# Performance work log

Measured on AMD Instinct MI355X. Metric: run time of the kernel, lower is better.

The kernel has to match this reference:

```python
import jax, jax.numpy as jnp
import numpy as np

B, OBS, H, A, E = 131072, 194, 64, 5, 3  # batch, obs dim, hidden, max_action_dim, n event types


def setup_inputs() -> dict:
    key = jax.random.key(0)
    ks = jax.random.split(key, 16)
    s = lambda k, shape, std=0.1: (jax.random.normal(k, shape, dtype=jnp.float32) * std)
    return {
        "x": jax.random.normal(ks[0], (B, OBS), dtype=jnp.float32),
        "action": jax.random.randint(ks[1], (B,), 0, A),
        "W1": s(ks[2], (OBS, H)), "b1": jnp.zeros((H,), jnp.float32),
        "W2": s(ks[3], (H, H)),   "b2": jnp.zeros((H,), jnp.float32),
        "Wh": s(ks[4], (E, H, A), 0.01), "bh": jnp.zeros((E, A), jnp.float32),
        "Wc1": s(ks[5], (OBS, H)), "bc1": jnp.zeros((H,), jnp.float32),
        "Wc2": s(ks[6], (H, H)),   "bc2": jnp.zeros((H,), jnp.float32),
        "Wc3": s(ks[7], (H, 1)),   "bc3": jnp.zeros((1,), jnp.float32),
    }


def reference(x, action, W1, b1, W2, b2, Wh, bh, Wc1, bc1, Wc2, bc2, Wc3, bc3):
    # shared trunk
    feat = jnp.tanh(jnp.tanh(x @ W1 + b1) @ W2 + b2)          # [B, H]
    # route each sample to one of E heads via argmax of first 3 obs dims
    ev = jnp.argmax(x[:, :E], axis=1)                          # [B] int
    all_logits = jnp.einsum('bh,eha->bea', feat, Wh) + bh      # [B, E, A]
    logits = jnp.take_along_axis(
        all_logits, jnp.broadcast_to(ev[:, None, None], (x.shape[0], 1, A)), axis=1
    )[:, 0]                                                    # [B, A]
    logp_all = jax.nn.log_softmax(logits, axis=-1)             # [B, A]
    logp = jnp.take_along_axis(logp_all, action[:, None], axis=1)[:, 0]  # [B]
    entropy = -jnp.sum(jnp.exp(logp_all) * logp_all, axis=-1)  # [B]
    # critic
    value = jnp.tanh(jnp.tanh(x @ Wc1 + bc1) @ Wc2 + bc2) @ Wc3 + bc3    # [B, 1]
    return action, logp, entropy, value
```

## Files before the change

### kernel.cpp

```cpp
#include <hip/hip_runtime.h>
#include <hip/hip_bf16.h>

constexpr int Bt    = 131072;
constexpr int OBS   = 194;

constexpr int W1B_S  = 0;
constexpr int WC1B_S = 14336;
constexpr int W2B_S  = 28672;
constexpr int WC2B_S = 36864;
constexpr int WHB_S  = 45056;
constexpr size_t EVG_B = 98304;
constexpr size_t HG_S  = 131072;

typedef short bf8   __attribute__((ext_vector_type(8)));
typedef float f32x4 __attribute__((ext_vector_type(4)));
typedef unsigned int u32;

__device__ __forceinline__ short f2bs(float f) {
    union { __hip_bfloat16 h; short s; } u;
    u.h = __float2bfloat16(f);
    return u.s;
}
__device__ __forceinline__ float bs2f(short s) {
    union { short s; __hip_bfloat16 h; } u;
    u.s = s;
    return __bfloat162float(u.h);
}
__device__ __forceinline__ u32 pk2(float a, float b) {
    union { __hip_bfloat162 h; u32 u; } r;
    r.h = __float22bfloat162_rn(float2{a, b});
    return r.u;
}
__device__ __forceinline__ float fast_tanh(float v) {
    v = fminf(fmaxf(v, -15.f), 15.f);
    float e = __expf(2.f * v);
    return (e - 1.f) * __builtin_amdgcn_rcpf(e + 1.f);
}
__device__ __forceinline__ void dma16(const void* g, void* s) {
    __builtin_amdgcn_global_load_lds(
        (const __attribute__((address_space(1))) u32*)g,
        (__attribute__((address_space(3))) u32*)s, 16, 0, 0);
}

__global__ void __launch_bounds__(256) prep(
    const float* __restrict__ W1, const float* __restrict__ b1,
    const float* __restrict__ W2, const float* __restrict__ Wh,
    const float* __restrict__ Wc1, const float* __restrict__ bc1,
    const float* __restrict__ Wc2, const float* __restrict__ Wc3,
    short* __restrict__ ws)
{
    const int gid = blockIdx.x * 256 + threadIdx.x;
    const int gsz = gridDim.x * 256;

    for (int i = gid; i < 14336; i += gsz) {
        int j = i & 7, l = (i >> 3) & 63, nt = (i >> 9) & 3, kb = i >> 11;
        int k = kb * 32 + ((l >> 4) << 3) + j;
        int n = nt * 16 + (l & 15);
        short v1 = 0, v2 = 0;
        if (k < OBS) {
            v1 = f2bs(W1[k * 64 + n]);
            v2 = f2bs(Wc1[k * 64 + n]);
        } else if (k == OBS) {
            v1 = f2bs(b1[n]);
            v2 = f2bs(bc1[n]);
        }
        ws[W1B_S + i]  = v1;
        ws[WC1B_S + i] = v2;
    }
    for (int i = gid; i < 8192; i += gsz) {
        int j = i & 7, l = (i >> 3) & 63, nt = (i >> 9) & 3, kb = i >> 11;
        int s = kb * 32 + ((l >> 4) << 3) + j;
        int kp = (s & 3) * 16 + (s >> 2);
        int n = nt * 16 + (l & 15);
        ws[W2B_S + i]  = f2bs(W2[kp * 64 + n]);
        ws[WC2B_S + i] = f2bs(Wc2[kp * 64 + n]);
    }
    for (int i = gid; i < 1024; i += gsz) {
        int j = i & 7, l = (i >> 3) & 63, kb = i >> 9;
        int s = kb * 32 + ((l >> 4) << 3) + j;
        int kp = (s & 3) * 16 + (s >> 2);
        int cc = l & 15;
        float v;
        if (cc == 15) v = Wc3[kp];
        else { int e = cc / 5, a = cc - 5 * e; v = Wh[(e * 64 + kp) * 5 + a]; }
        ws[WHB_S + i] = f2bs(v);
    }
}

constexpr int P1_XS0 = 57344;
constexpr int P1_XSS = 12544;
constexpr int P1_LDS = P1_XS0 + 8 * P1_XSS;

__global__ void __launch_bounds__(512, 2) trunk1(
    const float* __restrict__ x, const short* __restrict__ ws,
    short* __restrict__ hG, unsigned char* __restrict__ evG)
{
    __shared__ __align__(16) char smem[P1_LDS];
    const int t = threadIdx.x;
    const int l = t & 63, q = (t >> 4) & 3, c = t & 15;
    const int wu = __builtin_amdgcn_readfirstlane(t >> 6);

    #pragma unroll
    for (int i = 0; i < 7; ++i) {
        int ch = wu * 7 + i;
        dma16((const char*)ws + ch * 1024 + l * 16, smem + ch * 1024);
    }

    char* xs = smem + P1_XS0 + wu * P1_XSS;
    const int t0 = blockIdx.x * 32 + wu * 4;

    auto stage = [&](int tt) {
        const char* src = (const char*)x + (size_t)tt * 12416;
        #pragma unroll
        for (int ch = 0; ch < 12; ++ch)
            dma16(src + ch * 1024 + l * 16, xs + ch * 1024);
        dma16(src + 11392 + l * 16, xs + 11392);
    };
    stage(t0);

    __syncthreads();

    const bf8* fW1L  = reinterpret_cast<const bf8*>(smem);
    const bf8* fWc1L = reinterpret_cast<const bf8*>(smem + 28672);

    #pragma unroll 1
    for (int i = 0; i < 4; ++i) {
        const int tt = t0 + i;

        if (i) {
            asm volatile("s_waitcnt vmcnt(0)" ::: "memory");
            __builtin_amdgcn_sched_barrier(0);
        }

        union AF { u32 u[4]; bf8 v; } af[7];
        #pragma unroll
        for (int kb = 0; kb < 6; ++kb) {
            #pragma unroll
            for (int j = 0; j < 4; ++j) {
                float2 v = *reinterpret_cast<const float2*>(xs + c * 776 + kb * 128 + q * 32 + j * 8);
                af[kb].u[j] = pk2(v.x, v.y);
            }
        }
        af[6].u[0] = 0; af[6].u[1] = 0; af[6].u[2] = 0; af[6].u[3] = 0;
        if (q == 0) {
            float2 v = *reinterpret_cast<const float2*>(xs + c * 776 + 768);
            af[6].u[0] = pk2(v.x, v.y);
            af[6].u[1] = pk2(1.0f, 0.0f);
        }
        if (l < 16) {
            float2 v01 = *reinterpret_cast<const float2*>(xs + l * 776);
            float  v2  = *reinterpret_cast<const float*>(xs + l * 776 + 8);
            int ev = 0; float b = v01.x;
            if (v01.y > b) { b = v01.y; ev = 1; }
            if (v2 > b) ev = 2;
            evG[tt * 16 + l] = (unsigned char)ev;
        }

        __builtin_amdgcn_sched_barrier(0);
        if (i < 3) stage(tt + 1);
        __builtin_amdgcn_sched_barrier(0);

        f32x4 aa[4], ac[4];
        #pragma unroll
        for (int nt = 0; nt < 4; ++nt) {
            aa[nt] = f32x4{0.f, 0.f, 0.f, 0.f};
            ac[nt] = f32x4{0.f, 0.f, 0.f, 0.f};
        }
        #pragma unroll
        for (int kb = 0; kb < 7; ++kb) {
            bf8 a = af[kb].v;
            #pragma unroll
            for (int nt = 0; nt < 4; ++nt) {
                aa[nt] = __builtin_amdgcn_mfma_f32_16x16x32_bf16(a, fW1L [(kb * 4 + nt) * 64 + l], aa[nt], 0, 0, 0);
                ac[nt] = __builtin_amdgcn_mfma_f32_16x16x32_bf16(a, fWc1L[(kb * 4 + nt) * 64 + l], ac[nt], 0, 0, 0);
            }
        }
        short* hGt = hG + (size_t)tt * 2048;
        #pragma unroll
        for (int r = 0; r < 4; ++r) {
            uint2 pa, pc;
            pa.x = pk2(fast_tanh(aa[0][r]), fast_tanh(aa[1][r]));
            pa.y = pk2(fast_tanh(aa[2][r]), fast_tanh(aa[3][r]));
            pc.x = pk2(fast_tanh(ac[0][r]), fast_tanh(ac[1][r]));
            pc.y = pk2(fast_tanh(ac[2][r]), fast_tanh(ac[3][r]));
            *reinterpret_cast<uint2*>(hGt + (q * 4 + r) * 64 + 4 * c)        = pa;
            *reinterpret_cast<uint2*>(hGt + 1024 + (q * 4 + r) * 64 + 4 * c) = pc;
        }
    }
}

constexpr int F2_W   = 34816;
constexpr int F2_PW  = 5248;
constexpr int F2_LDS = F2_W + 8 * F2_PW;

__global__ void __launch_bounds__(512, 4) head2(
    const int* __restrict__ act_in,
    const float* __restrict__ b2, const float* __restrict__ bc2,
    const float* __restrict__ bh, const float* __restrict__ bc3,
    const short* __restrict__ ws,
    const short* __restrict__ hG, const unsigned char* __restrict__ evG,
    float* __restrict__ out)
{
    __shared__ __align__(16) char smem[F2_LDS];
    const int t = threadIdx.x;
    const int l = t & 63, q = (t >> 4) & 3, c = t & 15;
    const int wu = __builtin_amdgcn_readfirstlane(t >> 6);

    #pragma unroll
    for (int i = 0; i < 5; ++i) {
        int ch = wu + i * 8;
        if (ch < 34)
            dma16((const char*)ws + 57344 + ch * 1024 + l * 16, smem + ch * 1024);
    }

    float b2v[4], bc2v[4];
    #pragma unroll
    for (int nt = 0; nt < 4; ++nt) {
        b2v[nt]  = b2[nt * 16 + c];
        bc2v[nt] = bc2[nt * 16 + c];
    }
    float bhv = (c < 15) ? bh[c] : bc3[0];

    __syncthreads();

    const bf8* fW2L  = reinterpret_cast<const bf8*>(smem);
    const bf8* fWc2L = reinterpret_cast<const bf8*>(smem + 16384);
    const bf8* fWhL  = reinterpret_cast<const bf8*>(smem + 32768);
    short* ha = reinterpret_cast<short*>(smem + F2_W + wu * F2_PW);
    short* hc = ha + 1152;
    short* lw = reinterpret_cast<short*>(smem + F2_W + wu * F2_PW + 4608);
    float* vb = reinterpret_cast<float*>(smem + F2_W + wu * F2_PW + 5184);

    #pragma unroll 1
    for (int i = 0; i < 2; ++i) {
        const int tt = blockIdx.x * 16 + wu * 2 + i;
        const int gm = tt * 16 + c;
        int act = 0, evc = 0;
        if (l < 16) { act = act_in[gm]; evc = evG[gm]; }

        const short* hGt = hG + (size_t)tt * 2048;
        uint2 va[4], vc2[4];
        #pragma unroll
        for (int r = 0; r < 4; ++r) {
            va[r]  = *reinterpret_cast<const uint2*>(hGt + (q * 4 + r) * 64 + 4 * c);
            vc2[r] = *reinterpret_cast<const uint2*>(hGt + 1024 + (q * 4 + r) * 64 + 4 * c);
        }
        #pragma unroll
        for (int r = 0; r < 4; ++r) {
            *reinterpret_cast<uint2*>(&ha[(q * 4 + r) * 72 + 4 * c]) = va[r];
            *reinterpret_cast<uint2*>(&hc[(q * 4 + r) * 72 + 4 * c]) = vc2[r];
        }
        bf8 xa[2], xc[2];
        #pragma unroll
        for (int kb = 0; kb < 2; ++kb) {
            xa[kb] = *reinterpret_cast<const bf8*>(&ha[c * 72 + kb * 32 + q * 8]);
            xc[kb] = *reinterpret_cast<const bf8*>(&hc[c * 72 + kb * 32 + q * 8]);
        }

        f32x4 aa[4], ac[4];
        #pragma unroll
        for (int nt = 0; nt < 4; ++nt) {
            aa[nt] = f32x4{b2v[nt], b2v[nt], b2v[nt], b2v[nt]};
            ac[nt] = f32x4{bc2v[nt], bc2v[nt], bc2v[nt], bc2v[nt]};
        }
        #pragma unroll
        for (int kb = 0; kb < 2; ++kb) {
            #pragma unroll
            for (int nt = 0; nt < 4; ++nt) {
                aa[nt] = __builtin_amdgcn_mfma_f32_16x16x32_bf16(xa[kb], fW2L [(kb * 4 + nt) * 64 + l], aa[nt], 0, 0, 0);
                ac[nt] = __builtin_amdgcn_mfma_f32_16x16x32_bf16(xc[kb], fWc2L[(kb * 4 + nt) * 64 + l], ac[nt], 0, 0, 0);
            }
        }
        #pragma unroll
        for (int r = 0; r < 4; ++r) {
            uint2 pa, pc;
            pa.x = pk2(fast_tanh(aa[0][r]), fast_tanh(aa[1][r]));
            pa.y = pk2(fast_tanh(aa[2][r]), fast_tanh(aa[3][r]));
            pc.x = pk2(fast_tanh(ac[0][r]), fast_tanh(ac[1][r]));
            pc.y = pk2(fast_tanh(ac[2][r]), fast_tanh(ac[3][r]));
            *reinterpret_cast<uint2*>(&ha[(q * 4 + r) * 72 + 4 * c]) = pa;
            *reinterpret_cast<uint2*>(&hc[(q * 4 + r) * 72 + 4 * c]) = pc;
        }

        {
            f32x4 lg = f32x4{bhv, bhv, bhv, bhv};
            f32x4 vv = f32x4{bhv, bhv, bhv, bhv};
            #pragma unroll
            for (int kb = 0; kb < 2; ++kb) {
                bf8 bw = fWhL[kb * 64 + l];
                bf8 fa = *reinterpret_cast<const bf8*>(&ha[c * 72 + kb * 32 + q * 8]);
                bf8 fc = *reinterpret_cast<const bf8*>(&hc[c * 72 + kb * 32 + q * 8]);
                lg = __builtin_amdgcn_mfma_f32_16x16x32_bf16(fa, bw, lg, 0, 0, 0);
                vv = __builtin_amdgcn_mfma_f32_16x16x32_bf16(fc, bw, vv, 0, 0, 0);
            }
            #pragma unroll
            for (int r = 0; r < 4; ++r)
                lw[(q * 4 + r) * 18 + c] = f2bs(lg[r]);
            if (c == 15) {
                #pragma unroll
                for (int r = 0; r < 4; ++r)
                    vb[q * 4 + r] = vv[r];
            }
        }

        if (l < 16) {
            float lg[5];
            #pragma unroll
            for (int a = 0; a < 5; ++a)
                lg[a] = bs2f(lw[c * 18 + evc * 5 + a]);
            float mx = lg[0];
            #pragma unroll
            for (int a = 1; a < 5; ++a) mx = fmaxf(mx, lg[a]);
            float se = 0.f;
            #pragma unroll
            for (int a = 0; a < 5; ++a) se += __expf(lg[a] - mx);
            float lse = __logf(se) + mx;
            float lsel = lg[0];
            #pragma unroll
            for (int a = 1; a < 5; ++a) lsel = (act == a) ? lg[a] : lsel;
            float ent = 0.f;
            #pragma unroll
            for (int a = 0; a < 5; ++a) { float lp = lg[a] - lse; ent -= __expf(lp) * lp; }

            out[gm]          = (float)act;
            out[Bt + gm]     = lsel - lse;
            out[2 * Bt + gm] = ent;
            out[3 * Bt + gm] = vb[c];
        }
    }
}

extern "C" void kernel_launch(void* const* d_in, const int* in_sizes, int n_in,
                              void* d_out, int out_size, void* d_ws, size_t ws_size,
                              hipStream_t stream) {
    const float* x   = (const float*)d_in[0];
    const int*   act = (const int*)  d_in[1];
    const float* W1  = (const float*)d_in[2];
    const float* b1  = (const float*)d_in[3];
    const float* W2  = (const float*)d_in[4];
    const float* b2  = (const float*)d_in[5];
    const float* Wh  = (const float*)d_in[6];
    const float* bh  = (const float*)d_in[7];
    const float* Wc1 = (const float*)d_in[8];
    const float* bc1 = (const float*)d_in[9];
    const float* Wc2 = (const float*)d_in[10];
    const float* bc2 = (const float*)d_in[11];
    const float* Wc3 = (const float*)d_in[12];
    const float* bc3 = (const float*)d_in[13];
    float* out = (float*)d_out;
    short* ws  = (short*)d_ws;
    short* hG  = ws + HG_S;
    unsigned char* evG = (unsigned char*)d_ws + EVG_B;

    hipLaunchKernelGGL(prep, dim3(32), dim3(256), 0, stream,
                       W1, b1, W2, Wh, Wc1, bc1, Wc2, Wc3, ws);
    hipLaunchKernelGGL(trunk1, dim3(256), dim3(512), 0, stream,
                       x, ws, hG, evG);
    hipLaunchKernelGGL(head2, dim3(512), dim3(512), 0, stream,
                       act, b2, bc2, bh, bc3, ws, hG, evG, out);
}
```

Baseline: 199.5 us.

## Load x tiles directly into registers instead of LDS DMA staging in trunk1

The first-layer kernel no longer stages x rows into LDS with async DMA. Each lane now reads its float2 values straight from global memory into registers and prefetches the next tile while the MFMAs for the current tile run. LDS use drops to the weight buffer only, so launch bounds allow 4 blocks per CU and the grid doubles to 512 blocks of 2 tiles per wave. The trade-off is strided, less coalesced global loads per lane and higher register pressure from the prefetched raw buffer.

```diff
diff --git a/kernel.cpp b/kernel.cpp
--- a/kernel.cpp
+++ b/kernel.cpp
@@ -87,15 +87,11 @@
     }
 }
 
-constexpr int P1_XS0 = 57344;
-constexpr int P1_XSS = 12544;
-constexpr int P1_LDS = P1_XS0 + 8 * P1_XSS;
-
-__global__ void __launch_bounds__(512, 2) trunk1(
+__global__ void __launch_bounds__(512, 4) trunk1(
     const float* __restrict__ x, const short* __restrict__ ws,
     short* __restrict__ hG, unsigned char* __restrict__ evG)
 {
-    __shared__ __align__(16) char smem[P1_LDS];
+    __shared__ __align__(16) char smem[57344];
     const int t = threadIdx.x;
     const int l = t & 63, q = (t >> 4) & 3, c = t & 15;
     const int wu = __builtin_amdgcn_readfirstlane(t >> 6);
@@ -106,59 +102,53 @@
         dma16((const char*)ws + ch * 1024 + l * 16, smem + ch * 1024);
     }
 
-    char* xs = smem + P1_XS0 + wu * P1_XSS;
-    const int t0 = blockIdx.x * 32 + wu * 4;
-
-    auto stage = [&](int tt) {
-        const char* src = (const char*)x + (size_t)tt * 12416;
-        #pragma unroll
-        for (int ch = 0; ch < 12; ++ch)
-            dma16(src + ch * 1024 + l * 16, xs + ch * 1024);
-        dma16(src + 11392 + l * 16, xs + 11392);
-    };
-    stage(t0);
-
-    __syncthreads();
-
     const bf8* fW1L  = reinterpret_cast<const bf8*>(smem);
     const bf8* fWc1L = reinterpret_cast<const bf8*>(smem + 28672);
 
-    #pragma unroll 1
-    for (int i = 0; i < 4; ++i) {
-        const int tt = t0 + i;
-
-        if (i) {
-            asm volatile("s_waitcnt vmcnt(0)" ::: "memory");
-            __builtin_amdgcn_sched_barrier(0);
-        }
-
-        union AF { u32 u[4]; bf8 v; } af[7];
+    const int t0 = blockIdx.x * 16 + wu * 2;
+
+    float2 raw[24]; float2 rt6;
+    auto loadraw = [&](int tt) {
+        const float* xr = x + (size_t)tt * 16 * OBS + (size_t)c * OBS;
         #pragma unroll
         for (int kb = 0; kb < 6; ++kb) {
-            #pragma unroll
-            for (int j = 0; j < 4; ++j) {
-                float2 v = *reinterpret_cast<const float2*>(xs + c * 776 + kb * 128 + q * 32 + j * 8);
-                af[kb].u[j] = pk2(v.x, v.y);
-            }
+            const float2* p = reinterpret_cast<const float2*>(xr + kb * 32 + q * 8);
+            raw[kb * 4 + 0] = p[0]; raw[kb * 4 + 1] = p[1];
+            raw[kb * 4 + 2] = p[2]; raw[kb * 4 + 3] = p[3];
+        }
+        rt6 = float2{0.f, 0.f};
+        if (q == 0) rt6 = *reinterpret_cast<const float2*>(xr + 192);
+    };
+
+    union AF { u32 u[4]; bf8 v; } af[7];
+    auto packaf = [&](int tt) {
+        #pragma unroll
+        for (int kb = 0; kb < 6; ++kb) {
+            af[kb].u[0] = pk2(raw[kb * 4 + 0].x, raw[kb * 4 + 0].y);
+            af[kb].u[1] = pk2(raw[kb * 4 + 1].x, raw[kb * 4 + 1].y);
+            af[kb].u[2] = pk2(raw[kb * 4 + 2].x, raw[kb * 4 + 2].y);
+            af[kb].u[3] = pk2(raw[kb * 4 + 3].x, raw[kb * 4 + 3].y);
         }
         af[6].u[0] = 0; af[6].u[1] = 0; af[6].u[2] = 0; af[6].u[3] = 0;
         if (q == 0) {
-            float2 v = *reinterpret_cast<const float2*>(xs + c * 776 + 768);
-            af[6].u[0] = pk2(v.x, v.y);
+            af[6].u[0] = pk2(rt6.x, rt6.y);
             af[6].u[1] = pk2(1.0f, 0.0f);
         }
         if (l < 16) {
-            float2 v01 = *reinterpret_cast<const float2*>(xs + l * 776);
-            float  v2  = *reinterpret_cast<const float*>(xs + l * 776 + 8);
-            int ev = 0; float b = v01.x;
-            if (v01.y > b) { b = v01.y; ev = 1; }
-            if (v2 > b) ev = 2;
+            int ev = 0; float b = raw[0].x;
+            if (raw[0].y > b) { b = raw[0].y; ev = 1; }
+            if (raw[1].x > b) ev = 2;
             evG[tt * 16 + l] = (unsigned char)ev;
         }
-
-        __builtin_amdgcn_sched_barrier(0);
-        if (i < 3) stage(tt + 1);
-        __builtin_amdgcn_sched_barrier(0);
+    };
+
+    loadraw(t0);
+    __syncthreads();
+
+    #pragma unroll 1
+    for (int i = 0; i < 2; ++i) {
+        const int tt = t0 + i;
+        packaf(tt);
 
         f32x4 aa[4], ac[4];
         #pragma unroll
@@ -175,6 +165,9 @@
                 ac[nt] = __builtin_amdgcn_mfma_f32_16x16x32_bf16(a, fWc1L[(kb * 4 + nt) * 64 + l], ac[nt], 0, 0, 0);
             }
         }
+
+        if (i == 0) loadraw(t0 + 1);
+
         short* hGt = hG + (size_t)tt * 2048;
         #pragma unroll
         for (int r = 0; r < 4; ++r) {
@@ -354,7 +347,7 @@
 
     hipLaunchKernelGGL(prep, dim3(32), dim3(256), 0, stream,
                        W1, b1, W2, Wh, Wc1, bc1, Wc2, Wc3, ws);
-    hipLaunchKernelGGL(trunk1, dim3(256), dim3(512), 0, stream,
+    hipLaunchKernelGGL(trunk1, dim3(512), dim3(512), 0, stream,
                        x, ws, hG, evG);
     hipLaunchKernelGGL(head2, dim3(512), dim3(512), 0, stream,
                        act, b2, bc2, bh, bc3, ws, hG, evG, out);
```

New measurement: 311.5 us. 56.2% more time.
